# Performance work log

Measured on AMD Instinct MI355X. Metric: run time of the kernel, lower is better.

## Reference

```python
import jax, jax.numpy as jnp
import numpy as np

B, S, H, NH = 2, 2048, 1024, 16
HD = H // NH  # head_dim = 64


def setup_inputs() -> dict:
    key = jax.random.key(0)
    k1, k2, k3, k4, k5 = jax.random.split(key, 5)
    hidden_states = jax.random.normal(k1, (B, S, H), dtype=jnp.float32)
    # additive causal mask: 0 on/below diagonal, -1e9 above
    causal = jnp.tril(jnp.ones((S, S), dtype=jnp.bool_))
    attention_mask = jnp.where(causal, 0.0, -1e9).astype(jnp.float32)[None, None, :, :]
    scale = 0.02
    Wq = jax.random.normal(k2, (H, H), dtype=jnp.float32) * scale
    Wk = jax.random.normal(k3, (H, H), dtype=jnp.float32) * scale
    Wv = jax.random.normal(k4, (H, H), dtype=jnp.float32) * scale
    Wo = jax.random.normal(k5, (H, H), dtype=jnp.float32) * scale
    return {"hidden_states": hidden_states, "attention_mask": attention_mask,
            "Wq": Wq, "Wk": Wk, "Wv": Wv, "Wo": Wo}


def reference(hidden_states, attention_mask, Wq, Wk, Wv, Wo):
    b, s, _ = hidden_states.shape
    # nn.Linear: y = x @ W.T
    q = (hidden_states @ Wq.T).reshape(b, s, NH, HD).transpose(0, 2, 1, 3)  # [B,NH,S,HD]
    k = (hidden_states @ Wk.T).reshape(b, s, NH, HD).transpose(0, 2, 1, 3)
    v = (hidden_states @ Wv.T).reshape(b, s, NH, HD).transpose(0, 2, 1, 3)
    scores = jnp.einsum('bhqd,bhkd->bhqk', q, k) / jnp.sqrt(jnp.float32(HD))
    scores = scores + attention_mask
    attn = jax.nn.softmax(scores, axis=-1)
    out = jnp.einsum('bhqk,bhkd->bhqd', attn, v)  # [B,NH,S,HD]
    out = out.transpose(0, 2, 1, 3).reshape(b, s, H)
    return out @ Wo.T
```

## Files before the change

### kernel.cpp

```cpp
#include <hip/hip_runtime.h>
#include <hip/hip_bf16.h>

#define B_   2
#define S_   2048
#define H_   1024
#define NH_  16
#define HD_  64
#define MTOT 4096
#define KD   1024

typedef __attribute__((ext_vector_type(4)))  float    f32x4;
typedef __attribute__((ext_vector_type(16))) float    f32x16;
typedef __attribute__((ext_vector_type(8)))  short    bf16x8;
typedef __attribute__((ext_vector_type(2)))  unsigned u32x2;
typedef __attribute__((ext_vector_type(4)))  unsigned u32x4;

__device__ inline short f2bf(float x) {
    union { float f; unsigned u; } v; v.f = x;
    unsigned r = v.u + 0x7fffu + ((v.u >> 16) & 1u);
    return (short)(r >> 16);
}
__device__ inline unsigned pk2(float lo, float hi) {
    return (unsigned)(unsigned short)f2bf(lo) | ((unsigned)(unsigned short)f2bf(hi) << 16);
}
__device__ inline unsigned cvtpk(float lo, float hi) {
    unsigned r;
    asm("v_cvt_pk_bf16_f32 %0, %1, %2" : "=v"(r) : "v"(lo), "v"(hi));
    return r;
}
__device__ inline float max3f(float a, float b, float c) {
    float r;
    asm("v_max3_f32 %0, %1, %2, %3" : "=v"(r) : "v"(a), "v"(b), "v"(c));
    return r;
}
__device__ inline void gload16(const void* g, void* l) {
    __builtin_amdgcn_global_load_lds(
        (const __attribute__((address_space(1))) unsigned*)g,
        (__attribute__((address_space(3))) unsigned*)l, 16, 0, 0);
}

__global__ __launch_bounds__(256) void cvt_x(const float* __restrict__ x,
                                             unsigned* __restrict__ xb) {
    const size_t i = ((size_t)blockIdx.x * 256 + threadIdx.x) * 8;
    const f32x4 a = *(const f32x4*)(x + i);
    const f32x4 b = *(const f32x4*)(x + i + 4);
    u32x4 p;
    p[0] = pk2(a[0], a[1]); p[1] = pk2(a[2], a[3]);
    p[2] = pk2(b[0], b[1]); p[3] = pk2(b[2], b[3]);
    *(u32x4*)(xb + i / 2) = p;
}

__global__ __launch_bounds__(256) void wcvt(const float* __restrict__ W0,
                                            const float* __restrict__ W1,
                                            const float* __restrict__ W2,
                                            const float* __restrict__ W3,
                                            unsigned* __restrict__ wb) {
    const float* W = (blockIdx.y == 0) ? W0 : (blockIdx.y == 1) ? W1
                   : (blockIdx.y == 2) ? W2 : W3;
    const size_t i = ((size_t)blockIdx.x * 256 + threadIdx.x) * 8;
    const f32x4 a = *(const f32x4*)(W + i);
    const f32x4 b = *(const f32x4*)(W + i + 4);
    u32x4 p;
    p[0] = pk2(a[0], a[1]); p[1] = pk2(a[2], a[3]);
    p[2] = pk2(b[0], b[1]); p[3] = pk2(b[2], b[3]);
    *(u32x4*)(wb + (size_t)blockIdx.y * (H_ * KD / 2) + i / 2) = p;
}

template <int MODE>
__global__ __launch_bounds__(256) void gemm_m97(const short* __restrict__ A,
                                                const short* __restrict__ Wb,
                                                short* __restrict__ outb,
                                                float* __restrict__ outf) {
    __shared__ short Sm[128 * 128];
    short* As = Sm;
    short* Bs = Sm + 8192;

    const int tid = threadIdx.x, wave = tid >> 6, lane = tid & 63;
    const int wm = (wave >> 1) * 64, wn = (wave & 1) * 64;
    const int m0 = blockIdx.x * 128;

    int n0, widx;
    if constexpr (MODE == 0) {
        widx = blockIdx.y >> 3;
        n0 = (blockIdx.y & 7) * 128;
    } else {
        widx = 0;
        n0 = blockIdx.y * 128;
    }
    const short* W = Wb + (size_t)widx * H_ * KD;

    f32x4 acc[4][4] = {};

    for (int k0 = 0; k0 < KD; k0 += 64) {
#pragma unroll
        for (int c = 0; c < 4; ++c) {
            const int lin = wave * 4096 + c * 1024 + lane * 16;
            const int row = lin >> 7;
            const int col = (lin & 127) ^ ((row & 7) << 4);
            gload16(A + (size_t)(m0 + row) * KD + k0 + (col >> 1),
                    (char*)As + wave * 4096 + c * 1024);
            gload16(W + (size_t)(n0 + row) * KD + k0 + (col >> 1),
                    (char*)Bs + wave * 4096 + c * 1024);
        }
        __syncthreads();

#pragma unroll
        for (int ks = 0; ks < 2; ++ks) {
            bf16x8 af[4], bf[4];
#pragma unroll
            for (int i = 0; i < 4; ++i) {
                const int row = wm + i * 16 + (lane & 15);
                af[i] = *(const bf16x8*)((char*)As + row * 128 +
                        ((ks * 64 + (lane >> 4) * 16) ^ ((row & 7) << 4)));
            }
#pragma unroll
            for (int j = 0; j < 4; ++j) {
                const int row = wn + j * 16 + (lane & 15);
                bf[j] = *(const bf16x8*)((char*)Bs + row * 128 +
                        ((ks * 64 + (lane >> 4) * 16) ^ ((row & 7) << 4)));
            }
#pragma unroll
            for (int i = 0; i < 4; ++i)
#pragma unroll
                for (int j = 0; j < 4; ++j)
                    acc[i][j] = __builtin_amdgcn_mfma_f32_16x16x32_bf16(af[i], bf[j], acc[i][j], 0, 0, 0);
        }
        __syncthreads();
    }

    if constexpr (MODE == 0) {
#pragma unroll
        for (int i = 0; i < 4; ++i)
#pragma unroll
            for (int j = 0; j < 4; ++j)
#pragma unroll
                for (int r = 0; r < 4; ++r) {
                    const int mi = wm + i * 16 + (lane >> 4) * 4 + r;
                    const int ni = wn + j * 16 + (lane & 15);
                    const int byt = (mi * 256 + ni * 2) ^ ((mi & 7) << 4);
                    *(short*)((char*)Sm + byt) = f2bf(acc[i][j][r]);
                }
        __syncthreads();
        const int row = tid >> 1, half = tid & 1;
        const int m = m0 + row, bb = m >> 11, s = m & 2047;
        const int hh = (n0 >> 6) + half;
        short* dst = outb + (size_t)widx * MTOT * H_ +
                     (((size_t)(bb * NH_ + hh)) * S_ + s) * HD_;
#pragma unroll
        for (int k = 0; k < 8; ++k) {
            const int byt = (row * 256 + half * 128 + k * 16) ^ ((row & 7) << 4);
            *(bf16x8*)(dst + k * 8) = *(const bf16x8*)((char*)Sm + byt);
        }
    } else {
#pragma unroll
        for (int i = 0; i < 4; ++i)
#pragma unroll
            for (int j = 0; j < 4; ++j)
#pragma unroll
                for (int r = 0; r < 4; ++r) {
                    const int m = m0 + wm + i * 16 + (lane >> 4) * 4 + r;
                    const int n = n0 + wn + j * 16 + (lane & 15);
                    outf[(size_t)m * H_ + n] = acc[i][j][r];
                }
    }
}

__global__ __launch_bounds__(256) void flash2(const short* __restrict__ Qb,
                                              const short* __restrict__ Kb,
                                              const short* __restrict__ Vb,
                                              short* __restrict__ Ob) {
    const int bx = blockIdx.x;
    const int hi = bx >> 8, u = bx & 255;
    const int h = u >> 4, tq = u & 15;
    const int qt = hi ? (15 - tq) : tq;
    const int b  = hi;

    const int tid = threadIdx.x, wave = tid >> 6, lane = tid & 63;
    const int q0 = qt * 128;
    const int qw0 = q0 + wave * 32;
    const size_t hoff = ((size_t)(b * NH_ + h)) * S_ * HD_;
    const short* Q = Qb + hoff;
    const short* K = Kb + hoff;
    const short* V = Vb + hoff;

    __shared__ short Ks[2][64 * 64];
    __shared__ short Vt[2][64 * 64];

    const int ql = lane & 31;
    const int hh = lane >> 5;

    bf16x8 qf[4];
#pragma unroll
    for (int ds = 0; ds < 4; ++ds)
        qf[ds] = *(const bf16x8*)(Q + (size_t)(qw0 + ql) * HD_ + ds * 16 + hh * 8);

    f32x16 ot[2] = {};
    float mrun = -1e30f, lrun = 0.f;
    const float c2 = 0.18033688011112042f;

    const int kk = (tid & 31) * 2, d0v = (tid >> 5) * 8;
    bf16x8 vr0, vr1;
    auto stageK = [&](int kt, int buf) {
#pragma unroll
        for (int c = 0; c < 2; ++c) {
            const int lin = wave * 2048 + c * 1024 + lane * 16;
            const int row = lin >> 7;
            const int col = (lin & 127) ^ ((row & 7) << 4);
            gload16(K + (size_t)(kt * 64 + row) * HD_ + (col >> 1),
                    (char*)Ks[buf] + wave * 2048 + c * 1024);
        }
    };
    auto loadV = [&](int kt) {
        vr0 = *(const bf16x8*)(V + (size_t)(kt * 64 + kk) * HD_ + d0v);
        vr1 = *(const bf16x8*)(V + (size_t)(kt * 64 + kk + 1) * HD_ + d0v);
    };
    auto writeV = [&](int buf) {
#pragma unroll
        for (int i = 0; i < 8; ++i) {
            const int d = d0v + i;
            const int byt = d * 128 + kk * 2;
            *(unsigned*)((char*)Vt[buf] + (byt ^ ((d & 7) << 4))) =
                (unsigned)(unsigned short)vr0[i] | ((unsigned)(unsigned short)vr1[i] << 16);
        }
    };

    const int nkt = 2 * qt + 2;

    stageK(0, 0);
    loadV(0);
    writeV(0);
    __syncthreads();

    int cur = 0;
    for (int kt = 0; kt < nkt; ++kt) {
        const bool pre = (kt + 1 < nkt);
        if (pre) { stageK(kt + 1, cur ^ 1); loadV(kt + 1); }

        if (kt * 64 <= qw0 + 31) {
            const bool need_mask = (kt * 64 + 63) > qw0;

            f32x16 st[2] = {};
            __builtin_amdgcn_s_setprio(1);
#pragma unroll
            for (int t = 0; t < 2; ++t)
#pragma unroll
                for (int ds = 0; ds < 4; ++ds) {
                    const int row = t * 32 + ql;
                    const bf16x8 kf = *(const bf16x8*)((char*)Ks[cur] + row * 128 +
                            ((ds * 32 + hh * 16) ^ ((row & 7) << 4)));
                    st[t] = __builtin_amdgcn_mfma_f32_32x32x16_bf16(kf, qf[ds], st[t], 0, 0, 0);
                }
            __builtin_amdgcn_s_setprio(0);

            float sraw[32];
#pragma unroll
            for (int t = 0; t < 2; ++t)
#pragma unroll
                for (int r = 0; r < 16; ++r) {
                    float v = st[t][r];
                    if (need_mask) {
                        const int key = kt * 64 + t * 32 + (r & 3) + 8 * (r >> 2) + 4 * hh;
                        if (key > qw0 + ql) v = -1e30f;
                    }
                    sraw[t * 16 + r] = v;
                }

            float ma = fmaxf(sraw[0], sraw[1]);
            float mb = fmaxf(sraw[2], sraw[3]);
#pragma unroll
            for (int i = 4; i < 32; i += 4) {
                ma = max3f(ma, sraw[i],     sraw[i + 1]);
                mb = max3f(mb, sraw[i + 2], sraw[i + 3]);
            }
            const float pmax = fmaxf(fmaxf(ma, mb), __shfl_xor(fmaxf(ma, mb), 32, 64));

            if (!__all((pmax - mrun) <= 44.36f)) {
                const float mnew = fmaxf(mrun, pmax);
                const float corr = exp2f((mrun - mnew) * c2);
                mrun = mnew;
                lrun *= corr;
#pragma unroll
                for (int dt = 0; dt < 2; ++dt)
#pragma unroll
                    for (int r = 0; r < 16; ++r) ot[dt][r] *= corr;
            }
            const float mc = mrun * c2;

            float p[32];
#pragma unroll
            for (int i = 0; i < 32; ++i) p[i] = exp2f(fmaf(sraw[i], c2, -mc));
            float ts[16];
#pragma unroll
            for (int i = 0; i < 16; ++i) ts[i] = p[i] + p[i + 16];
#pragma unroll
            for (int stp = 8; stp >= 1; stp >>= 1)
#pragma unroll
                for (int i = 0; i < 8; ++i)
                    if (i < stp) ts[i] += ts[i + stp];
            lrun += ts[0] + __shfl_xor(ts[0], 32, 64);

#pragma unroll
            for (int ks = 0; ks < 4; ++ks) {
                const int t = ks >> 1, rb = (ks & 1) * 8;
                const unsigned a0 = cvtpk(p[t * 16 + rb + 0], p[t * 16 + rb + 1]);
                const unsigned a1 = cvtpk(p[t * 16 + rb + 2], p[t * 16 + rb + 3]);
                const unsigned a2 = cvtpk(p[t * 16 + rb + 4], p[t * 16 + rb + 5]);
                const unsigned a3 = cvtpk(p[t * 16 + rb + 6], p[t * 16 + rb + 7]);
                const unsigned s0 = __shfl_xor(a0, 32, 64);
                const unsigned s1 = __shfl_xor(a1, 32, 64);
                const unsigned s2 = __shfl_xor(a2, 32, 64);
                const unsigned s3 = __shfl_xor(a3, 32, 64);
                u32x4 pw;
                pw[0] = hh ? s2 : a0;
                pw[1] = hh ? s3 : a1;
                pw[2] = hh ? a2 : s0;
                pw[3] = hh ? a3 : s1;
                const bf16x8 pf = __builtin_bit_cast(bf16x8, pw);
                __builtin_amdgcn_s_setprio(1);
#pragma unroll
                for (int dt = 0; dt < 2; ++dt) {
                    const int row = dt * 32 + ql;
                    const bf16x8 vf = *(const bf16x8*)((char*)Vt[cur] + row * 128 +
                            ((ks * 32 + hh * 16) ^ ((row & 7) << 4)));
                    ot[dt] = __builtin_amdgcn_mfma_f32_32x32x16_bf16(vf, pf, ot[dt], 0, 0, 0);
                }
                __builtin_amdgcn_s_setprio(0);
            }
        }

        if (pre) writeV(cur ^ 1);
        __syncthreads();
        cur ^= 1;
    }

    const float inv = 1.f / lrun;
    short* orow = Ob + ((size_t)(b * S_) + q0 + wave * 32 + ql) * H_ + h * HD_;
#pragma unroll
    for (int dt = 0; dt < 2; ++dt)
#pragma unroll
        for (int g4 = 0; g4 < 4; ++g4) {
            const int dbase = dt * 32 + 8 * g4 + 4 * hh;
            u32x2 w;
            w[0] = cvtpk(ot[dt][g4 * 4 + 0] * inv, ot[dt][g4 * 4 + 1] * inv);
            w[1] = cvtpk(ot[dt][g4 * 4 + 2] * inv, ot[dt][g4 * 4 + 3] * inv);
            *(u32x2*)(orow + dbase) = w;
        }
}

extern "C" void kernel_launch(void* const* d_in, const int* in_sizes, int n_in,
                              void* d_out, int out_size, void* d_ws, size_t ws_size,
                              hipStream_t stream) {
    const float* x  = (const float*)d_in[0];
    const float* Wq = (const float*)d_in[2];
    const float* Wk = (const float*)d_in[3];
    const float* Wv = (const float*)d_in[4];
    const float* Wo = (const float*)d_in[5];
    float* out = (float*)d_out;

    short* qkv = (short*)d_ws;
    short* xb  = qkv + (size_t)3 * MTOT * H_;
    short* wb  = xb + (size_t)MTOT * H_;

    cvt_x<<<2048, 256, 0, stream>>>(x, (unsigned*)xb);
    wcvt<<<dim3(512, 4), 256, 0, stream>>>(Wq, Wk, Wv, Wo, (unsigned*)wb);

    gemm_m97<0><<<dim3(32, 24), 256, 0, stream>>>(xb, wb, qkv, nullptr);

    flash2<<<dim3(512), 256, 0, stream>>>(
        qkv, qkv + (size_t)MTOT * H_, qkv + (size_t)2 * MTOT * H_, xb);

    gemm_m97<1><<<dim3(32, 8), 256, 0, stream>>>(
        xb, wb + (size_t)3 * H_ * KD, nullptr, out);
}
```

Baseline: 152.0 us.

## Split attention KV range across two wave groups and merge partial softmax results

The flash attention kernel now runs 512 threads per block, with two groups of four waves each handling half of the causal key tiles for the same query tile. Each group uses its own double-buffered K/V shared memory. At the end the second group writes its partial output and running max/sum to shared memory, and the first group merges them with rescaled weights. This shortens the serial KV loop per block and adds in-block parallelism, at the cost of more shared memory, an extra merge step and register pressure from launch bounds.

```diff
diff --git a/kernel.cpp b/kernel.cpp
--- a/kernel.cpp
+++ b/kernel.cpp
@@ -165,10 +165,10 @@
     }
 }
 
-__global__ __launch_bounds__(256) void flash2(const short* __restrict__ Qb,
-                                              const short* __restrict__ Kb,
-                                              const short* __restrict__ Vb,
-                                              short* __restrict__ Ob) {
+__global__ __launch_bounds__(512, 4) void flash3(const short* __restrict__ Qb,
+                                                 const short* __restrict__ Kb,
+                                                 const short* __restrict__ Vb,
+                                                 short* __restrict__ Ob) {
     const int bx = blockIdx.x;
     const int hi = bx >> 8, u = bx & 255;
     const int h = u >> 4, tq = u & 15;
@@ -176,15 +176,17 @@
     const int b  = hi;
 
     const int tid = threadIdx.x, wave = tid >> 6, lane = tid & 63;
+    const int qg = wave & 3, half = wave >> 2;
+    const int th = tid & 255;
     const int q0 = qt * 128;
-    const int qw0 = q0 + wave * 32;
+    const int qw0 = q0 + qg * 32;
     const size_t hoff = ((size_t)(b * NH_ + h)) * S_ * HD_;
     const short* Q = Qb + hoff;
     const short* K = Kb + hoff;
     const short* V = Vb + hoff;
 
-    __shared__ short Ks[2][64 * 64];
-    __shared__ short Vt[2][64 * 64];
+    __shared__ short Ks[2][2][4096];
+    __shared__ short Vt[2][2][4096];
 
     const int ql = lane & 31;
     const int hh = lane >> 5;
@@ -198,16 +200,16 @@
     float mrun = -1e30f, lrun = 0.f;
     const float c2 = 0.18033688011112042f;
 
-    const int kk = (tid & 31) * 2, d0v = (tid >> 5) * 8;
+    const int kk = (th & 31) * 2, d0v = (th >> 5) * 8;
     bf16x8 vr0, vr1;
     auto stageK = [&](int kt, int buf) {
 #pragma unroll
         for (int c = 0; c < 2; ++c) {
-            const int lin = wave * 2048 + c * 1024 + lane * 16;
+            const int lin = qg * 2048 + c * 1024 + lane * 16;
             const int row = lin >> 7;
             const int col = (lin & 127) ^ ((row & 7) << 4);
             gload16(K + (size_t)(kt * 64 + row) * HD_ + (col >> 1),
-                    (char*)Ks[buf] + wave * 2048 + c * 1024);
+                    (char*)Ks[half][buf] + qg * 2048 + c * 1024);
         }
     };
     auto loadV = [&](int kt) {
@@ -219,21 +221,23 @@
         for (int i = 0; i < 8; ++i) {
             const int d = d0v + i;
             const int byt = d * 128 + kk * 2;
-            *(unsigned*)((char*)Vt[buf] + (byt ^ ((d & 7) << 4))) =
+            *(unsigned*)((char*)Vt[half][buf] + (byt ^ ((d & 7) << 4))) =
                 (unsigned)(unsigned short)vr0[i] | ((unsigned)(unsigned short)vr1[i] << 16);
         }
     };
 
-    const int nkt = 2 * qt + 2;
-
-    stageK(0, 0);
-    loadV(0);
+    const int niter = qt + 1;
+    const int ktbase = half ? (qt + 1) : 0;
+
+    stageK(ktbase, 0);
+    loadV(ktbase);
     writeV(0);
     __syncthreads();
 
     int cur = 0;
-    for (int kt = 0; kt < nkt; ++kt) {
-        const bool pre = (kt + 1 < nkt);
+    for (int it = 0; it < niter; ++it) {
+        const int kt = ktbase + it;
+        const bool pre = (it + 1 < niter);
         if (pre) { stageK(kt + 1, cur ^ 1); loadV(kt + 1); }
 
         if (kt * 64 <= qw0 + 31) {
@@ -246,7 +250,7 @@
 #pragma unroll
                 for (int ds = 0; ds < 4; ++ds) {
                     const int row = t * 32 + ql;
-                    const bf16x8 kf = *(const bf16x8*)((char*)Ks[cur] + row * 128 +
+                    const bf16x8 kf = *(const bf16x8*)((char*)Ks[half][cur] + row * 128 +
                             ((ds * 32 + hh * 16) ^ ((row & 7) << 4)));
                     st[t] = __builtin_amdgcn_mfma_f32_32x32x16_bf16(kf, qf[ds], st[t], 0, 0, 0);
                 }
@@ -320,7 +324,7 @@
 #pragma unroll
                 for (int dt = 0; dt < 2; ++dt) {
                     const int row = dt * 32 + ql;
-                    const bf16x8 vf = *(const bf16x8*)((char*)Vt[cur] + row * 128 +
+                    const bf16x8 vf = *(const bf16x8*)((char*)Vt[half][cur] + row * 128 +
                             ((ks * 32 + hh * 16) ^ ((row & 7) << 4)));
                     ot[dt] = __builtin_amdgcn_mfma_f32_32x32x16_bf16(vf, pf, ot[dt], 0, 0, 0);
                 }
@@ -333,18 +337,51 @@
         cur ^= 1;
     }
 
-    const float inv = 1.f / lrun;
-    short* orow = Ob + ((size_t)(b * S_) + q0 + wave * 32 + ql) * H_ + h * HD_;
-#pragma unroll
-    for (int dt = 0; dt < 2; ++dt)
-#pragma unroll
-        for (int g4 = 0; g4 < 4; ++g4) {
-            const int dbase = dt * 32 + 8 * g4 + 4 * hh;
-            u32x2 w;
-            w[0] = cvtpk(ot[dt][g4 * 4 + 0] * inv, ot[dt][g4 * 4 + 1] * inv);
-            w[1] = cvtpk(ot[dt][g4 * 4 + 2] * inv, ot[dt][g4 * 4 + 3] * inv);
-            *(u32x2*)(orow + dbase) = w;
-        }
+    float* Osh = (float*)Ks;
+    float* Msh = (float*)Vt;
+    const int swz = (lane & 7) << 2;
+
+    if (half == 1) {
+        float* dst = Osh + ((size_t)qg * 64 + lane) * 32;
+#pragma unroll
+        for (int dt = 0; dt < 2; ++dt)
+#pragma unroll
+            for (int g4 = 0; g4 < 4; ++g4) {
+                f32x4 t;
+                t[0] = ot[dt][g4 * 4 + 0]; t[1] = ot[dt][g4 * 4 + 1];
+                t[2] = ot[dt][g4 * 4 + 2]; t[3] = ot[dt][g4 * 4 + 3];
+                *(f32x4*)(dst + ((dt * 16 + g4 * 4) ^ swz)) = t;
+            }
+        Msh[(qg * 64 + lane) * 2 + 0] = mrun;
+        Msh[(qg * 64 + lane) * 2 + 1] = lrun;
+    }
+    __syncthreads();
+
+    if (half == 0) {
+        const float* src = Osh + ((size_t)qg * 64 + lane) * 32;
+        const float mB = Msh[(qg * 64 + lane) * 2 + 0];
+        const float lB = Msh[(qg * 64 + lane) * 2 + 1];
+        const float m  = fmaxf(mrun, mB);
+        const float al = exp2f((mrun - m) * c2);
+        const float be = exp2f((mB   - m) * c2);
+        const float inv = 1.f / (al * lrun + be * lB);
+        const float ai = al * inv, bi = be * inv;
+
+        short* orow = Ob + ((size_t)(b * S_) + q0 + qg * 32 + ql) * H_ + h * HD_;
+#pragma unroll
+        for (int dt = 0; dt < 2; ++dt)
+#pragma unroll
+            for (int g4 = 0; g4 < 4; ++g4) {
+                const f32x4 ob = *(const f32x4*)(src + ((dt * 16 + g4 * 4) ^ swz));
+                const int dbase = dt * 32 + 8 * g4 + 4 * hh;
+                u32x2 w;
+                w[0] = cvtpk(ot[dt][g4 * 4 + 0] * ai + ob[0] * bi,
+                             ot[dt][g4 * 4 + 1] * ai + ob[1] * bi);
+                w[1] = cvtpk(ot[dt][g4 * 4 + 2] * ai + ob[2] * bi,
+                             ot[dt][g4 * 4 + 3] * ai + ob[3] * bi);
+                *(u32x2*)(orow + dbase) = w;
+            }
+    }
 }
 
 extern "C" void kernel_launch(void* const* d_in, const int* in_sizes, int n_in,
@@ -366,7 +403,7 @@
 
     gemm_m97<0><<<dim3(32, 24), 256, 0, stream>>>(xb, wb, qkv, nullptr);
 
-    flash2<<<dim3(512), 256, 0, stream>>>(
+    flash3<<<dim3(512), 512, 0, stream>>>(
         qkv, qkv + (size_t)MTOT * H_, qkv + (size_t)2 * MTOT * H_, xb);
 
     gemm_m97<1><<<dim3(32, 8), 256, 0, stream>>>(
```

Measured after the change: 153.0 us. About the same (+0.6%).

## Store V transposed from QKV GEMM and stream K/V directly from global in attention

Applied to the files above, without the earlier changes.

The QKV GEMM epilogue now writes V in a [b,h,d,s] transposed layout, so attention no longer has to transpose V through LDS. The attention kernel drops shared-memory staging, double buffering and the per-tile __syncthreads. Each wave loads its K and V^T fragments straight from global or L2 into registers and runs only its own causal iterations, with launch bounds set for 3 blocks per CU. This removes LDS traffic and barriers, but every wave now re-reads K/V independently, and the transposed V store writes strided 8-byte chunks.

```diff
diff --git a/kernel.cpp b/kernel.cpp
--- a/kernel.cpp
+++ b/kernel.cpp
@@ -12,6 +12,7 @@
 typedef __attribute__((ext_vector_type(4)))  float    f32x4;
 typedef __attribute__((ext_vector_type(16))) float    f32x16;
 typedef __attribute__((ext_vector_type(8)))  short    bf16x8;
+typedef __attribute__((ext_vector_type(4)))  short    bf16x4;
 typedef __attribute__((ext_vector_type(2)))  unsigned u32x2;
 typedef __attribute__((ext_vector_type(4)))  unsigned u32x4;
 
@@ -129,27 +130,44 @@
     }
 
     if constexpr (MODE == 0) {
-#pragma unroll
-        for (int i = 0; i < 4; ++i)
-#pragma unroll
-            for (int j = 0; j < 4; ++j)
-#pragma unroll
-                for (int r = 0; r < 4; ++r) {
-                    const int mi = wm + i * 16 + (lane >> 4) * 4 + r;
-                    const int ni = wn + j * 16 + (lane & 15);
-                    const int byt = (mi * 256 + ni * 2) ^ ((mi & 7) << 4);
-                    *(short*)((char*)Sm + byt) = f2bf(acc[i][j][r]);
+        if (widx == 2) {
+#pragma unroll
+            for (int i = 0; i < 4; ++i)
+#pragma unroll
+                for (int j = 0; j < 4; ++j) {
+                    const int m = m0 + wm + i * 16 + (lane >> 4) * 4;
+                    const int n = n0 + wn + j * 16 + (lane & 15);
+                    const int bb = m >> 11, s = m & 2047;
+                    const int hd = n >> 6, d = n & 63;
+                    bf16x4 w;
+#pragma unroll
+                    for (int r = 0; r < 4; ++r) w[r] = f2bf(acc[i][j][r]);
+                    *(bf16x4*)(outb + (size_t)2 * MTOT * H_ +
+                               (((size_t)(bb * NH_ + hd)) * HD_ + d) * S_ + s) = w;
                 }
-        __syncthreads();
-        const int row = tid >> 1, half = tid & 1;
-        const int m = m0 + row, bb = m >> 11, s = m & 2047;
-        const int hh = (n0 >> 6) + half;
-        short* dst = outb + (size_t)widx * MTOT * H_ +
-                     (((size_t)(bb * NH_ + hh)) * S_ + s) * HD_;
-#pragma unroll
-        for (int k = 0; k < 8; ++k) {
-            const int byt = (row * 256 + half * 128 + k * 16) ^ ((row & 7) << 4);
-            *(bf16x8*)(dst + k * 8) = *(const bf16x8*)((char*)Sm + byt);
+        } else {
+#pragma unroll
+            for (int i = 0; i < 4; ++i)
+#pragma unroll
+                for (int j = 0; j < 4; ++j)
+#pragma unroll
+                    for (int r = 0; r < 4; ++r) {
+                        const int mi = wm + i * 16 + (lane >> 4) * 4 + r;
+                        const int ni = wn + j * 16 + (lane & 15);
+                        const int byt = (mi * 256 + ni * 2) ^ ((mi & 7) << 4);
+                        *(short*)((char*)Sm + byt) = f2bf(acc[i][j][r]);
+                    }
+            __syncthreads();
+            const int row = tid >> 1, half = tid & 1;
+            const int m = m0 + row, bb = m >> 11, s = m & 2047;
+            const int hh = (n0 >> 6) + half;
+            short* dst = outb + (size_t)widx * MTOT * H_ +
+                         (((size_t)(bb * NH_ + hh)) * S_ + s) * HD_;
+#pragma unroll
+            for (int k = 0; k < 8; ++k) {
+                const int byt = (row * 256 + half * 128 + k * 16) ^ ((row & 7) << 4);
+                *(bf16x8*)(dst + k * 8) = *(const bf16x8*)((char*)Sm + byt);
+            }
         }
     } else {
 #pragma unroll
@@ -165,26 +183,23 @@
     }
 }
 
-__global__ __launch_bounds__(256) void flash2(const short* __restrict__ Qb,
-                                              const short* __restrict__ Kb,
-                                              const short* __restrict__ Vb,
-                                              short* __restrict__ Ob) {
+__global__ __launch_bounds__(256, 3) void flash5(const short* __restrict__ Qb,
+                                                 const short* __restrict__ Kb,
+                                                 const short* __restrict__ Vtb,
+                                                 short* __restrict__ Ob) {
     const int bx = blockIdx.x;
     const int hi = bx >> 8, u = bx & 255;
     const int h = u >> 4, tq = u & 15;
     const int qt = hi ? (15 - tq) : tq;
     const int b  = hi;
 
-    const int tid = threadIdx.x, wave = tid >> 6, lane = tid & 63;
+    const int tid = threadIdx.x, qg = tid >> 6, lane = tid & 63;
     const int q0 = qt * 128;
-    const int qw0 = q0 + wave * 32;
+    const int qw0 = q0 + qg * 32;
     const size_t hoff = ((size_t)(b * NH_ + h)) * S_ * HD_;
-    const short* Q = Qb + hoff;
-    const short* K = Kb + hoff;
-    const short* V = Vb + hoff;
-
-    __shared__ short Ks[2][64 * 64];
-    __shared__ short Vt[2][64 * 64];
+    const short* Q  = Qb  + hoff;
+    const short* K  = Kb  + hoff;
+    const short* Vt = Vtb + hoff;
 
     const int ql = lane & 31;
     const int hh = lane >> 5;
@@ -198,143 +213,108 @@
     float mrun = -1e30f, lrun = 0.f;
     const float c2 = 0.18033688011112042f;
 
-    const int kk = (tid & 31) * 2, d0v = (tid >> 5) * 8;
-    bf16x8 vr0, vr1;
-    auto stageK = [&](int kt, int buf) {
-#pragma unroll
-        for (int c = 0; c < 2; ++c) {
-            const int lin = wave * 2048 + c * 1024 + lane * 16;
-            const int row = lin >> 7;
-            const int col = (lin & 127) ^ ((row & 7) << 4);
-            gload16(K + (size_t)(kt * 64 + row) * HD_ + (col >> 1),
-                    (char*)Ks[buf] + wave * 2048 + c * 1024);
-        }
-    };
-    auto loadV = [&](int kt) {
-        vr0 = *(const bf16x8*)(V + (size_t)(kt * 64 + kk) * HD_ + d0v);
-        vr1 = *(const bf16x8*)(V + (size_t)(kt * 64 + kk + 1) * HD_ + d0v);
-    };
-    auto writeV = [&](int buf) {
-#pragma unroll
-        for (int i = 0; i < 8; ++i) {
-            const int d = d0v + i;
-            const int byt = d * 128 + kk * 2;
-            *(unsigned*)((char*)Vt[buf] + (byt ^ ((d & 7) << 4))) =
-                (unsigned)(unsigned short)vr0[i] | ((unsigned)(unsigned short)vr1[i] << 16);
-        }
-    };
-
-    const int nkt = 2 * qt + 2;
-
-    stageK(0, 0);
-    loadV(0);
-    writeV(0);
-    __syncthreads();
-
-    int cur = 0;
-    for (int kt = 0; kt < nkt; ++kt) {
-        const bool pre = (kt + 1 < nkt);
-        if (pre) { stageK(kt + 1, cur ^ 1); loadV(kt + 1); }
-
-        if (kt * 64 <= qw0 + 31) {
-            const bool need_mask = (kt * 64 + 63) > qw0;
-
-            f32x16 st[2] = {};
+    const int niter = (qw0 + 95) >> 6;
+    for (int kt = 0; kt < niter; ++kt) {
+        bf16x8 kf[2][4];
+#pragma unroll
+        for (int t = 0; t < 2; ++t)
+#pragma unroll
+            for (int ds = 0; ds < 4; ++ds)
+                kf[t][ds] = *(const bf16x8*)(K + (size_t)(kt * 64 + t * 32 + ql) * HD_ +
+                                             ds * 16 + hh * 8);
+
+        f32x16 st[2] = {};
+        __builtin_amdgcn_s_setprio(1);
+#pragma unroll
+        for (int t = 0; t < 2; ++t)
+#pragma unroll
+            for (int ds = 0; ds < 4; ++ds)
+                st[t] = __builtin_amdgcn_mfma_f32_32x32x16_bf16(kf[t][ds], qf[ds], st[t], 0, 0, 0);
+        __builtin_amdgcn_s_setprio(0);
+
+        bf16x8 vf[2][4];
+#pragma unroll
+        for (int dt = 0; dt < 2; ++dt)
+#pragma unroll
+            for (int ks = 0; ks < 4; ++ks)
+                vf[dt][ks] = *(const bf16x8*)(Vt + (size_t)(dt * 32 + ql) * S_ +
+                                              kt * 64 + ks * 16 + hh * 8);
+
+        const bool need_mask = (kt * 64 + 63) > qw0;
+        float sraw[32];
+#pragma unroll
+        for (int t = 0; t < 2; ++t)
+#pragma unroll
+            for (int r = 0; r < 16; ++r) {
+                float v = st[t][r];
+                if (need_mask) {
+                    const int key = kt * 64 + t * 32 + (r & 3) + 8 * (r >> 2) + 4 * hh;
+                    if (key > qw0 + ql) v = -1e30f;
+                }
+                sraw[t * 16 + r] = v;
+            }
+
+        float ma = fmaxf(sraw[0], sraw[1]);
+        float mb = fmaxf(sraw[2], sraw[3]);
+#pragma unroll
+        for (int i = 4; i < 32; i += 4) {
+            ma = max3f(ma, sraw[i],     sraw[i + 1]);
+            mb = max3f(mb, sraw[i + 2], sraw[i + 3]);
+        }
+        const float pmax = fmaxf(fmaxf(ma, mb), __shfl_xor(fmaxf(ma, mb), 32, 64));
+
+        if (!__all((pmax - mrun) <= 44.36f)) {
+            const float mnew = fmaxf(mrun, pmax);
+            const float corr = exp2f((mrun - mnew) * c2);
+            mrun = mnew;
+            lrun *= corr;
+#pragma unroll
+            for (int dt = 0; dt < 2; ++dt)
+#pragma unroll
+                for (int r = 0; r < 16; ++r) ot[dt][r] *= corr;
+        }
+        const float mc = mrun * c2;
+
+        float p[32];
+#pragma unroll
+        for (int i = 0; i < 32; ++i) p[i] = exp2f(fmaf(sraw[i], c2, -mc));
+        float ts[16];
+#pragma unroll
+        for (int i = 0; i < 16; ++i) ts[i] = p[i] + p[i + 16];
+#pragma unroll
+        for (int stp = 8; stp >= 1; stp >>= 1)
+#pragma unroll
+            for (int i = 0; i < 8; ++i)
+                if (i < stp) ts[i] += ts[i + stp];
+        lrun += ts[0] + __shfl_xor(ts[0], 32, 64);
+
+#pragma unroll
+        for (int ks = 0; ks < 4; ++ks) {
+            const int t = ks >> 1, rb = (ks & 1) * 8;
+            const unsigned a0 = cvtpk(p[t * 16 + rb + 0], p[t * 16 + rb + 1]);
+            const unsigned a1 = cvtpk(p[t * 16 + rb + 2], p[t * 16 + rb + 3]);
+            const unsigned a2 = cvtpk(p[t * 16 + rb + 4], p[t * 16 + rb + 5]);
+            const unsigned a3 = cvtpk(p[t * 16 + rb + 6], p[t * 16 + rb + 7]);
+            const unsigned s0 = __shfl_xor(a0, 32, 64);
+            const unsigned s1 = __shfl_xor(a1, 32, 64);
+            const unsigned s2 = __shfl_xor(a2, 32, 64);
+            const unsigned s3 = __shfl_xor(a3, 32, 64);
+            u32x4 pw;
+            pw[0] = hh ? s2 : a0;
+            pw[1] = hh ? s3 : a1;
+            pw[2] = hh ? a2 : s0;
+            pw[3] = hh ? a3 : s1;
+            const bf16x8 pf = __builtin_bit_cast(bf16x8, pw);
             __builtin_amdgcn_s_setprio(1);
 #pragma unroll
-            for (int t = 0; t < 2; ++t)
-#pragma unroll
-                for (int ds = 0; ds < 4; ++ds) {
-                    const int row = t * 32 + ql;
-                    const bf16x8 kf = *(const bf16x8*)((char*)Ks[cur] + row * 128 +
-                            ((ds * 32 + hh * 16) ^ ((row & 7) << 4)));
-                    st[t] = __builtin_amdgcn_mfma_f32_32x32x16_bf16(kf, qf[ds], st[t], 0, 0, 0);
-                }
+            for (int dt = 0; dt < 2; ++dt)
+                ot[dt] = __builtin_amdgcn_mfma_f32_32x32x16_bf16(vf[dt][ks], pf, ot[dt], 0, 0, 0);
             __builtin_amdgcn_s_setprio(0);
-
-            float sraw[32];
-#pragma unroll
-            for (int t = 0; t < 2; ++t)
-#pragma unroll
-                for (int r = 0; r < 16; ++r) {
-                    float v = st[t][r];
-                    if (need_mask) {
-                        const int key = kt * 64 + t * 32 + (r & 3) + 8 * (r >> 2) + 4 * hh;
-                        if (key > qw0 + ql) v = -1e30f;
-                    }
-                    sraw[t * 16 + r] = v;
-                }
-
-            float ma = fmaxf(sraw[0], sraw[1]);
-            float mb = fmaxf(sraw[2], sraw[3]);
-#pragma unroll
-            for (int i = 4; i < 32; i += 4) {
-                ma = max3f(ma, sraw[i],     sraw[i + 1]);
-                mb = max3f(mb, sraw[i + 2], sraw[i + 3]);
-            }
-            const float pmax = fmaxf(fmaxf(ma, mb), __shfl_xor(fmaxf(ma, mb), 32, 64));
-
-            if (!__all((pmax - mrun) <= 44.36f)) {
-                const float mnew = fmaxf(mrun, pmax);
-                const float corr = exp2f((mrun - mnew) * c2);
-                mrun = mnew;
-                lrun *= corr;
-#pragma unroll
-                for (int dt = 0; dt < 2; ++dt)
-#pragma unroll
-                    for (int r = 0; r < 16; ++r) ot[dt][r] *= corr;
-            }
-            const float mc = mrun * c2;
-
-            float p[32];
-#pragma unroll
-            for (int i = 0; i < 32; ++i) p[i] = exp2f(fmaf(sraw[i], c2, -mc));
-            float ts[16];
-#pragma unroll
-            for (int i = 0; i < 16; ++i) ts[i] = p[i] + p[i + 16];
-#pragma unroll
-            for (int stp = 8; stp >= 1; stp >>= 1)
-#pragma unroll
-                for (int i = 0; i < 8; ++i)
-                    if (i < stp) ts[i] += ts[i + stp];
-            lrun += ts[0] + __shfl_xor(ts[0], 32, 64);
-
-#pragma unroll
-            for (int ks = 0; ks < 4; ++ks) {
-                const int t = ks >> 1, rb = (ks & 1) * 8;
-                const unsigned a0 = cvtpk(p[t * 16 + rb + 0], p[t * 16 + rb + 1]);
-                const unsigned a1 = cvtpk(p[t * 16 + rb + 2], p[t * 16 + rb + 3]);
-                const unsigned a2 = cvtpk(p[t * 16 + rb + 4], p[t * 16 + rb + 5]);
-                const unsigned a3 = cvtpk(p[t * 16 + rb + 6], p[t * 16 + rb + 7]);
-                const unsigned s0 = __shfl_xor(a0, 32, 64);
-                const unsigned s1 = __shfl_xor(a1, 32, 64);
-                const unsigned s2 = __shfl_xor(a2, 32, 64);
-                const unsigned s3 = __shfl_xor(a3, 32, 64);
-                u32x4 pw;
-                pw[0] = hh ? s2 : a0;
-                pw[1] = hh ? s3 : a1;
-                pw[2] = hh ? a2 : s0;
-                pw[3] = hh ? a3 : s1;
-                const bf16x8 pf = __builtin_bit_cast(bf16x8, pw);
-                __builtin_amdgcn_s_setprio(1);
-#pragma unroll
-                for (int dt = 0; dt < 2; ++dt) {
-                    const int row = dt * 32 + ql;
-                    const bf16x8 vf = *(const bf16x8*)((char*)Vt[cur] + row * 128 +
-                            ((ks * 32 + hh * 16) ^ ((row & 7) << 4)));
-                    ot[dt] = __builtin_amdgcn_mfma_f32_32x32x16_bf16(vf, pf, ot[dt], 0, 0, 0);
-                }
-                __builtin_amdgcn_s_setprio(0);
-            }
-        }
-
-        if (pre) writeV(cur ^ 1);
-        __syncthreads();
-        cur ^= 1;
+        }
     }
 
     const float inv = 1.f / lrun;
-    short* orow = Ob + ((size_t)(b * S_) + q0 + wave * 32 + ql) * H_ + h * HD_;
+    short* orow = Ob + ((size_t)(b * S_) + q0 + qg * 32 + ql) * H_ + h * HD_;
 #pragma unroll
     for (int dt = 0; dt < 2; ++dt)
 #pragma unroll
@@ -366,7 +346,7 @@
 
     gemm_m97<0><<<dim3(32, 24), 256, 0, stream>>>(xb, wb, qkv, nullptr);
 
-    flash2<<<dim3(512), 256, 0, stream>>>(
+    flash5<<<dim3(512), 256, 0, stream>>>(
         qkv, qkv + (size_t)MTOT * H_, qkv + (size_t)2 * MTOT * H_, xb);
 
     gemm_m97<1><<<dim3(32, 8), 256, 0, stream>>>(
```

Result: faster. 148.5 us (-2.3%).
